# Kernel tuning notes

Measured on AMD Instinct MI355X. Metric: run time of the kernel, lower is better.

Reference implementation:

```python
import jax, jax.numpy as jnp
from jax import lax
import numpy as np

Z, Y, X = 41, 256, 256  # sparse_shape = grid_size[::-1]
N_VOX = 60000
C_IN = 4
DN = ('NCDHW', 'OIDHW', 'NCDHW')


def _conv(x, w, stride=(1, 1, 1), pad=1):
    return lax.conv_general_dilated(x, w, stride, [(pad, pad)] * 3, dimension_numbers=DN)


def _tconv(x, w, stride=(2, 2, 2), pad=1, outpad=(0, 0, 0)):
    # torch ConvTranspose3d (weight [Cin,Cout,k,k,k]) == conv with lhs dilation,
    # spatially-flipped, in/out-swapped kernel, padding (k-1-p, k-1-p+output_padding)
    wt = jnp.flip(jnp.swapaxes(w, 0, 1), axis=(2, 3, 4))
    padding = [(2 - pad, 2 - pad + op) for op in outpad]  # k=3
    return lax.conv_general_dilated(x, wt, (1, 1, 1), padding, lhs_dilation=stride, dimension_numbers=DN)


def _bn_relu(y, s, b, m):
    # eval-mode BN folded into per-channel scale/shift, then ReLU, then restrict
    # to the sparse active-site mask (spconv only stores features at active sites)
    return jax.nn.relu(y * s[None, :, None, None, None] + b[None, :, None, None, None]) * m


def _forward(feats, params, coords, batch_size):
    (w1, s1, b1, w2a, s2a, b2a, w2b, s2b, b2b, w3a, s3a, b3a, w3b, s3b, b3b,
     w4a, s4a, b4a, w4b, s4b, b4b, w5a, s5a, b5a, w5b, s5b, b5b) = params
    B = batch_size
    bi, zi, yi, xi = coords[:, 0], coords[:, 1], coords[:, 2], coords[:, 3]
    dense = jnp.zeros((B, C_IN, Z, Y, X), feats.dtype).at[bi, :, zi, yi, xi].set(feats)
    m0 = jnp.zeros((B, 1, Z, Y, X), feats.dtype).at[bi, 0, zi, yi, xi].set(1.0)
    one = jnp.ones((1, 1, 3, 3, 3), feats.dtype)
    # conv1: SparseConv3d k3 s1 p1 -> active set dilates
    m1 = (_conv(m0, one) > 0).astype(feats.dtype)
    x = _bn_relu(_conv(dense, w1), s1, b1, m1)
    # conv2: SparseConv3d s2 + SubMConv3d (mask unchanged for subm)
    m2 = (_conv(m1, one, (2, 2, 2)) > 0).astype(feats.dtype)
    x = _bn_relu(_conv(x, w2a, (2, 2, 2)), s2a, b2a, m2)
    x = _bn_relu(_conv(x, w2b), s2b, b2b, m2)
    # conv3
    m3 = (_conv(m2, one, (2, 2, 2)) > 0).astype(feats.dtype)
    x = _bn_relu(_conv(x, w3a, (2, 2, 2)), s3a, b3a, m3)
    x = _bn_relu(_conv(x, w3b), s3b, b3b, m3)
    # deconv4: SparseConvTranspose3d s2 + subm
    m4 = (_tconv(m3, one) > 0).astype(feats.dtype)
    x = _bn_relu(_tconv(x, w4a), s4a, b4a, m4)
    x = _bn_relu(_conv(x, w4b), s4b, b4b, m4)
    # deconv5: output_padding (0,3,3) restores full Y/X resolution
    m5 = (_tconv(m4, one, outpad=(0, 3, 3)) > 0).astype(feats.dtype)
    x = _bn_relu(_tconv(x, w5a, outpad=(0, 3, 3)), s5a, b5a, m5)
    x = _bn_relu(_conv(x, w5b), s5b, b5b, m5)
    return x  # dense [B, 32, Z, Y, X]; zeros at inactive sites


def setup_inputs() -> dict:
    rng = np.random.default_rng(0)
    flat = rng.choice(Z * Y * X, size=N_VOX, replace=False)
    zi = (flat // (Y * X)).astype(np.int32)
    rem = flat % (Y * X)
    yi = (rem // X).astype(np.int32)
    xi = (rem % X).astype(np.int32)
    coords = np.stack([np.zeros(N_VOX, np.int32), zi, yi, xi], axis=1)

    def w(o, i):
        return jnp.asarray((rng.standard_normal((o, i, 3, 3, 3)) * 0.05).astype(np.float32))

    def scale(c):
        return jnp.asarray(rng.uniform(0.5, 1.5, c).astype(np.float32))

    def shift(c):
        return jnp.asarray((rng.standard_normal(c) * 0.1).astype(np.float32))

    return {
        'occ_voxel_features': jnp.asarray(rng.standard_normal((N_VOX, C_IN)).astype(np.float32)),
        'occ_voxel_coords': jnp.asarray(coords),
        'batch_size': 1,
        'w1': w(16, 4), 's1': scale(16), 'b1': shift(16),
        'w2a': w(32, 16), 's2a': scale(32), 'b2a': shift(32),
        'w2b': w(32, 32), 's2b': scale(32), 'b2b': shift(32),
        'w3a': w(64, 32), 's3a': scale(64), 'b3a': shift(64),
        'w3b': w(64, 64), 's3b': scale(64), 'b3b': shift(64),
        'w4a': w(64, 32), 's4a': scale(32), 'b4a': shift(32),  # transpose weight [Cin,Cout,...]
        'w4b': w(32, 32), 's4b': scale(32), 'b4b': shift(32),
        'w5a': w(32, 32), 's5a': scale(32), 'b5a': shift(32),
        'w5b': w(32, 32), 's5b': scale(32), 'b5b': shift(32),
    }


def reference(occ_voxel_features, occ_voxel_coords, batch_size,
              w1, s1, b1, w2a, s2a, b2a, w2b, s2b, b2b,
              w3a, s3a, b3a, w3b, s3b, b3b,
              w4a, s4a, b4a, w4b, s4b, b4b,
              w5a, s5a, b5a, w5b, s5b, b5b):
    params = (w1, s1, b1, w2a, s2a, b2a, w2b, s2b, b2b, w3a, s3a, b3a, w3b, s3b, b3b,
              w4a, s4a, b4a, w4b, s4b, b4b, w5a, s5a, b5a, w5b, s5b, b5b)
    return _forward(occ_voxel_features, params, occ_voxel_coords, batch_size)
```

## Files before the change

### kernel.cpp

```cpp
#include <hip/hip_runtime.h>
#include <hip/hip_bf16.h>
#include <stdint.h>

namespace {

constexpr int Z0 = 41, Y0 = 256, X0 = 256;
constexpr int Z2 = 21, Y2 = 128, X2 = 128;
constexpr int Z3 = 11, Y3 = 64,  X3 = 64;
constexpr int Z4 = 21, Y4 = 127, X4 = 127;
constexpr int NV0 = Z0 * Y0 * X0;
constexpr int NV2 = Z2 * Y2 * X2;
constexpr int NV3 = Z3 * Y3 * X3;
constexpr int NV4 = Z4 * Y4 * X4;

constexpr int ZP0 = 43, YP0 = 258, XP0 = 258; constexpr int NP0 = ZP0 * YP0 * XP0;
constexpr int ZP2 = 23, YP2 = 130, XP2 = 130; constexpr int NP2 = ZP2 * YP2 * XP2;
constexpr int ZP3 = 13, YP3 = 66,  XP3 = 66;  constexpr int NP3 = ZP3 * YP3 * XP3;
constexpr int ZP4 = 23, YP4 = 129, XP4 = 129; constexpr int NP4 = ZP4 * YP4 * XP4;

using bf16 = __hip_bfloat16;
typedef __attribute__((ext_vector_type(8))) short s16x8;
typedef __attribute__((ext_vector_type(4))) float f32x4;
typedef __attribute__((ext_vector_type(16))) float f32x16;
typedef __attribute__((ext_vector_type(4))) unsigned u32x4;

__device__ inline unsigned f2b(float f) {
    return (unsigned)__builtin_bit_cast(unsigned short, __float2bfloat16(f));
}

__device__ inline int xcd_swz(int bid, int nwg) {
    int q = nwg >> 3, r = nwg & 7;
    int x = bid & 7, j = bid >> 3;
    return (x < r ? x * (q + 1) : r * (q + 1) + (x - r) * q) + j;
}

__device__ inline void glds16(const bf16* g, void* l) {
    __builtin_amdgcn_global_load_lds(
        (const __attribute__((address_space(1))) void*)g,
        (__attribute__((address_space(3))) void*)l, 16, 0, 0);
}

__global__ __launch_bounds__(256) void sentinel_k(float* out) { out[0] = 12345.0f; }

__global__ __launch_bounds__(256) void scatter_k(const float* __restrict__ feats,
                                                 const int* __restrict__ coords,
                                                 bf16* __restrict__ dense,
                                                 uint8_t* __restrict__ m0, int n) {
    int v = blockIdx.x * 256 + threadIdx.x;
    if (v >= n) return;
    int z = coords[v * 4 + 1], y = coords[v * 4 + 2], x = coords[v * 4 + 3];
    m0[(z * Y0 + y) * X0 + x] = 1;
    int pp = ((z + 1) * YP0 + (y + 1)) * XP0 + (x + 1);
    uint2 u;
    u.x = f2b(feats[v * 4 + 0]) | (f2b(feats[v * 4 + 1]) << 16);
    u.y = f2b(feats[v * 4 + 2]) | (f2b(feats[v * 4 + 3]) << 16);
    *(uint2*)(dense + (size_t)pp * 4) = u;
}

template <int C>
__global__ __launch_bounds__(256) void halo_zero_k(bf16* __restrict__ buf,
                                                   int Zi, int Yi, int Xi,
                                                   int Zp, int Yp, int Xp) {
    int i = blockIdx.x * 256 + threadIdx.x;
    int tot = Zp * Yp * Xp;
    if (i >= tot) return;
    int x = i % Xp; int t = i / Xp; int y = t % Yp; int z = t / Yp;
    bool halo = (z < 1) | (z > Zi) | (y < 1) | (y > Yi) | (x < 1) | (x > Xi);
    if (!halo) return;
    uint4 zz = make_uint4(0, 0, 0, 0);
    uint4* p = (uint4*)(buf + (size_t)i * C);
#pragma unroll
    for (int j = 0; j < C / 8; ++j) p[j] = zz;
}

__global__ __launch_bounds__(256) void repack_frag_k(const float* __restrict__ w,
                                                     bf16* __restrict__ wf,
                                                     int CIN, int COUT, int TRANS) {
    int NT = COUT / 16, KT = CIN / 32;
    int i = blockIdx.x * 256 + threadIdx.x;
    int total = 27 * NT * KT * 64;
    if (i >= total) return;
    int lane = i & 63; int t = i >> 6;
    int kt = t % KT; t /= KT; int nt = t % NT; int tap = t / NT;
    int co = nt * 16 + (lane & 15);
    int ci0 = kt * 32 + (lane >> 4) * 8;
    unsigned e[8];
#pragma unroll
    for (int j = 0; j < 8; ++j) {
        int ci = ci0 + j;
        int src = TRANS ? ((ci * COUT + co) * 27 + tap) : ((co * CIN + ci) * 27 + tap);
        e[j] = f2b(w[src]);
    }
    uint4 u;
    u.x = e[0] | (e[1] << 16); u.y = e[2] | (e[3] << 16);
    u.z = e[4] | (e[5] << 16); u.w = e[6] | (e[7] << 16);
    ((uint4*)wf)[i] = u;
}

__global__ __launch_bounds__(256) void repack_frag32_k(const float* __restrict__ w,
                                                       bf16* __restrict__ wf) {
    int i = blockIdx.x * 256 + threadIdx.x;
    if (i >= 27 * 2 * 64) return;
    int lane = i & 63; int t2 = i >> 6;
    int ks = t2 & 1; int tap = t2 >> 1;
    int co = lane & 31; int h = lane >> 5;
    unsigned e[8];
#pragma unroll
    for (int j = 0; j < 8; ++j) {
        int cin = ks * 16 + h * 8 + j;
        e[j] = f2b(w[(co * 32 + cin) * 27 + tap]);
    }
    uint4 u;
    u.x = e[0] | (e[1] << 16); u.y = e[2] | (e[3] << 16);
    u.z = e[4] | (e[5] << 16); u.w = e[6] | (e[7] << 16);
    ((uint4*)wf)[i] = u;
}

__global__ __launch_bounds__(256) void repack_frag_c16_k(const float* __restrict__ w,
                                                         bf16* __restrict__ wf) {
    int i = blockIdx.x * 256 + threadIdx.x;
    int total = 14 * 2 * 64;
    if (i >= total) return;
    int lane = i & 63; int t = i >> 6;
    int nt = t & 1; int p = t >> 1;
    int lg = lane >> 4, lr = lane & 15;
    int co = nt * 16 + lr;
    unsigned e[8];
#pragma unroll
    for (int j = 0; j < 8; ++j) {
        int tap = 2 * p + (lg >> 1);
        int ci = (lg & 1) * 8 + j;
        e[j] = (tap < 27) ? f2b(w[(co * 16 + ci) * 27 + tap]) : 0u;
    }
    uint4 u;
    u.x = e[0] | (e[1] << 16); u.y = e[2] | (e[3] << 16);
    u.z = e[4] | (e[5] << 16); u.w = e[6] | (e[7] << 16);
    ((uint4*)wf)[i] = u;
}

__global__ __launch_bounds__(256) void repack_frag_l1_k(const float* __restrict__ w,
                                                        bf16* __restrict__ wf) {
    int i = blockIdx.x * 256 + threadIdx.x;
    if (i >= 256) return;
    int lane = i & 63, kb = i >> 6;
    int lg = lane >> 4, lr = lane & 15;
    unsigned e[8];
#pragma unroll
    for (int j = 0; j < 8; ++j) {
        int tap = kb * 8 + lg * 2 + (j >> 2);
        int ci = j & 3;
        e[j] = (tap < 27) ? f2b(w[(lr * 4 + ci) * 27 + tap]) : 0u;
    }
    uint4 u;
    u.x = e[0] | (e[1] << 16); u.y = e[2] | (e[3] << 16);
    u.z = e[4] | (e[5] << 16); u.w = e[6] | (e[7] << 16);
    ((uint4*)wf)[i] = u;
}

__global__ __launch_bounds__(256) void dilate_k(const uint8_t* __restrict__ in,
                                                uint8_t* __restrict__ out,
                                                int Zi, int Yi, int Xi,
                                                int Zo, int Yo, int Xo, int stride) {
    int idx = blockIdx.x * 256 + threadIdx.x;
    int total = Zo * Yo * Xo;
    if (idx >= total) return;
    int x = idx % Xo; int t = idx / Xo; int y = t % Yo; int z = t / Yo;
    int YX = Yi * Xi;
    uint8_t r = 0;
    for (int kz = 0; kz < 3; ++kz) {
        int zi = z * stride + kz - 1;
        if ((unsigned)zi >= (unsigned)Zi) continue;
        for (int ky = 0; ky < 3; ++ky) {
            int yi = y * stride + ky - 1;
            if ((unsigned)yi >= (unsigned)Yi) continue;
            for (int kx = 0; kx < 3; ++kx) {
                int xi = x * stride + kx - 1;
                if ((unsigned)xi >= (unsigned)Xi) continue;
                r |= in[zi * YX + yi * Xi + xi];
            }
        }
    }
    out[idx] = r ? 1 : 0;
}

__global__ __launch_bounds__(256) void dilate4_k(const uint8_t* __restrict__ in,
                                                 uint8_t* __restrict__ out,
                                                 int Z, int Y, int X) {
    int ngx = X >> 2;
    int g = blockIdx.x * 256 + threadIdx.x;
    int total = Z * Y * ngx;
    if (g >= total) return;
    int gx = g % ngx; int t = g / ngx; int y = t % Y; int z = t / Y;
    const int YX = Y * X;
    unsigned r = 0;
    for (int kz = 0; kz < 3; ++kz) {
        int zi = z + kz - 1;
        if ((unsigned)zi >= (unsigned)Z) continue;
        for (int ky = 0; ky < 3; ++ky) {
            int yi = y + ky - 1;
            if ((unsigned)yi >= (unsigned)Y) continue;
            const unsigned* rw = (const unsigned*)(in + zi * YX + yi * X);
            unsigned u1 = rw[gx];
            unsigned u0 = gx ? rw[gx - 1] : 0u;
            unsigned u2 = (gx + 1 < ngx) ? rw[gx + 1] : 0u;
            r |= u1 | ((u1 << 8) | (u0 >> 24)) | ((u1 >> 8) | (u2 << 24));
        }
    }
    r |= r >> 4; r |= r >> 2; r |= r >> 1; r &= 0x01010101u;
    ((unsigned*)out)[g] = r;
}

__global__ __launch_bounds__(256) void tdilate_k(const uint8_t* __restrict__ in,
                                                 uint8_t* __restrict__ out,
                                                 int Zi, int Yi, int Xi,
                                                 int Zo, int Yo, int Xo) {
    int idx = blockIdx.x * 256 + threadIdx.x;
    int total = Zo * Yo * Xo;
    if (idx >= total) return;
    int x = idx % Xo; int t = idx / Xo; int y = t % Yo; int z = t / Yo;
    int YX = Yi * Xi;
    uint8_t r = 0;
    for (int kz = 0; kz < 3; ++kz) {
        int tz = z + 1 - kz;
        if (tz & 1) continue;
        int zi = tz >> 1;
        if ((unsigned)zi >= (unsigned)Zi) continue;
        for (int ky = 0; ky < 3; ++ky) {
            int ty = y + 1 - ky;
            if (ty & 1) continue;
            int yi = ty >> 1;
            if ((unsigned)yi >= (unsigned)Yi) continue;
            for (int kx = 0; kx < 3; ++kx) {
                int tx = x + 1 - kx;
                if (tx & 1) continue;
                int xi = tx >> 1;
                if ((unsigned)xi >= (unsigned)Xi) continue;
                r |= in[zi * YX + yi * Xi + xi];
            }
        }
    }
    out[idx] = r ? 1 : 0;
}

__global__ __launch_bounds__(256) void tdilate4_k(const uint8_t* __restrict__ in,
                                                  uint8_t* __restrict__ out,
                                                  int Zi, int Yi, int Xi,
                                                  int Zo, int Yo, int Xo) {
    int ngx = Xo >> 2;
    int g = blockIdx.x * 256 + threadIdx.x;
    int total = Zo * Yo * ngx;
    if (g >= total) return;
    int gx = g % ngx; int t = g / ngx; int y = t % Yo; int z = t / Yo;
    int YX = Yi * Xi;
    int j0 = gx * 2;
    unsigned r0 = 0, r1 = 0, r2 = 0, r3 = 0;
    for (int kz = 0; kz < 3; ++kz) {
        int tz = z + 1 - kz;
        if (tz & 1) continue;
        int zi = tz >> 1;
        if ((unsigned)zi >= (unsigned)Zi) continue;
        for (int ky = 0; ky < 3; ++ky) {
            int ty = y + 1 - ky;
            if (ty & 1) continue;
            int yi = ty >> 1;
            if ((unsigned)yi >= (unsigned)Yi) continue;
            const uint8_t* rp = in + zi * YX + yi * Xi;
            unsigned b0 = (j0 < Xi) ? rp[j0] : 0u;
            unsigned b1 = (j0 + 1 < Xi) ? rp[j0 + 1] : 0u;
            unsigned b2 = (j0 + 2 < Xi) ? rp[j0 + 2] : 0u;
            r0 |= b0; r1 |= b0 | b1; r2 |= b1; r3 |= b1 | b2;
        }
    }
    unsigned rr = (r0 ? 1u : 0u) | (r1 ? 0x100u : 0u) | (r2 ? 0x10000u : 0u) | (r3 ? 0x1000000u : 0u);
    ((unsigned*)out)[g] = rr;
}

__global__ __launch_bounds__(512, 2) void conv_roll_k(
    const bf16* __restrict__ in, const bf16* __restrict__ wfrag,
    const float* __restrict__ scale, const float* __restrict__ shift,
    const uint8_t* __restrict__ mask, float* __restrict__ outf) {
    constexpr int ROWB = 2176;
    constexpr int SLABB = 24576;
    __shared__ uint4 ring4[5 * SLABB / 16];
    char* ring = (char*)ring4;

    const int bid = xcd_swz(blockIdx.x, gridDim.x);
    const int tx = bid & 7, ty = bid >> 3;
    const int y0 = ty * 8, x0 = tx * 32;

    const int tid = threadIdx.x;
    const int w = tid >> 6, lane = tid & 63;
    const int vx = lane & 31, h = lane >> 5;
    const int yr = w;

#pragma unroll
    for (int k = 0; k < 7; ++k) {
        int i = tid + k * 512;
        if (i < 27 * 2 * 64) {
            glds16(wfrag + (size_t)(k * 512 + w * 64 + lane) * 8,
                   ring + (k * 512 + w * 64) * 16);
        }
    }
    asm volatile("s_waitcnt vmcnt(0)" ::: "memory");
    __syncthreads();

    u32x4 breg[27][2];
#pragma unroll
    for (int t = 0; t < 27; ++t) {
        breg[t][0] = *(const u32x4*)(ring + (t * 2 + 0) * 1024 + lane * 16);
        breg[t][1] = *(const u32x4*)(ring + (t * 2 + 1) * 1024 + lane * 16);
    }
    __syncthreads();

    int soff[3];
#pragma unroll
    for (int k = 0; k < 3; ++k) {
        int i = tid + k * 512;
        int ii = i < 1360 ? i : 0;
        int row = ii / 136, c = ii - row * 136;
        int ks = c / 68, r2 = c - ks * 68, hh = r2 / 34, v = r2 - hh * 34;
        soff[k] = ((y0 + row) * XP0 + (x0 + v)) * 32 + (2 * ks + hh) * 8;
    }
    auto stagefn = [&](int p, char* slab) {
        int zs = p < ZP0 ? p : ZP0 - 1;
        const bf16* pb = in + (size_t)zs * ((size_t)YP0 * XP0 * 32);
        glds16(pb + soff[0], slab + w * 1024);
        glds16(pb + soff[1], slab + w * 1024 + 8192);
        glds16(pb + soff[2], slab + w * 1024 + 16384);
    };

    int asw[3];
#pragma unroll
    for (int dx = 0; dx < 3; ++dx) asw[dx] = h * 544 + (vx + dx) * 16;

    const float sc = scale[vx], sh = shift[vx];

    stagefn(0, ring);
    stagefn(1, ring + SLABB);
    stagefn(2, ring + 2 * SLABB);
    stagefn(3, ring + 3 * SLABB);
    stagefn(4, ring + 4 * SLABB);
    asm volatile("s_waitcnt vmcnt(0)" ::: "memory");
    __builtin_amdgcn_s_barrier();

    int s0 = 0;
    for (int z = 0; z < Z0; ++z) {
        const int s1 = s0 + 1 < 5 ? s0 + 1 : 0;
        const int s2 = s1 + 1 < 5 ? s1 + 1 : 0;
        const char* sl0 = ring + s0 * SLABB;
        const char* sl1 = ring + s1 * SLABB;
        const char* sl2 = ring + s2 * SLABB;

        f32x16 acc;
#pragma unroll
        for (int i = 0; i < 16; ++i) acc[i] = 0.f;

#pragma unroll
        for (int dz = 0; dz < 3; ++dz) {
            const char* slab = dz == 0 ? sl0 : (dz == 1 ? sl1 : sl2);
#pragma unroll
            for (int dy = 0; dy < 3; ++dy) {
                const char* rowp = slab + (yr + dy) * ROWB;
#pragma unroll
                for (int dx = 0; dx < 3; ++dx) {
                    const int tap = dz * 9 + dy * 3 + dx;
                    u32x4 a0 = *(const u32x4*)(rowp + asw[dx]);
                    u32x4 a1 = *(const u32x4*)(rowp + 1088 + asw[dx]);
                    acc = __builtin_amdgcn_mfma_f32_32x32x16_bf16(
                        __builtin_bit_cast(s16x8, a0),
                        __builtin_bit_cast(s16x8, breg[tap][0]), acc, 0, 0, 0);
                    acc = __builtin_amdgcn_mfma_f32_32x32x16_bf16(
                        __builtin_bit_cast(s16x8, a1),
                        __builtin_bit_cast(s16x8, breg[tap][1]), acc, 0, 0, 0);
                }
            }
        }

        const uint8_t* mrow = mask + ((size_t)z * Y0 + (y0 + yr)) * X0 + x0 + 4 * h;
        unsigned mq0 = *(const unsigned*)(mrow);
        unsigned mq1 = *(const unsigned*)(mrow + 8);
        unsigned mq2 = *(const unsigned*)(mrow + 16);
        unsigned mq3 = *(const unsigned*)(mrow + 24);

        const size_t obase = (size_t)vx * NV0 + ((size_t)z * Y0 + (y0 + yr)) * X0 + x0 + 4 * h;
#pragma unroll
        for (int q = 0; q < 4; ++q) {
            unsigned mq = q == 0 ? mq0 : (q == 1 ? mq1 : (q == 2 ? mq2 : mq3));
            f32x4 o;
#pragma unroll
            for (int r = 0; r < 4; ++r) {
                float m = (float)((mq >> (8 * r)) & 1);
                o[r] = fmaxf(fmaf(acc[q * 4 + r], sc, sh), 0.f) * m;
            }
            *(f32x4*)(outf + obase + 8 * q) = o;
        }

        __builtin_amdgcn_s_barrier();
        stagefn(z + 5, ring + s0 * SLABB);
        asm volatile("s_waitcnt vmcnt(11)" ::: "memory");
        s0 = s1;
    }
}

__global__ __launch_bounds__(256, 3) void tconv_roll_k(
    const bf16* __restrict__ in, const bf16* __restrict__ wfrag,
    const float* __restrict__ scale, const float* __restrict__ shift,
    const uint8_t* __restrict__ mask, bf16* __restrict__ out,
    int Zo, int Yo, int Xo, int Zi, int Ypi, int Xpi, int Ypo, int Xpo, int nx) {
    constexpr int ROWB = 34 * 64;
    constexpr int SLABB = 3 * ROWB;
    __shared__ uint4 ring4[4 * SLABB / 16];
    char* ring = (char*)ring4;

    const int oct = blockIdx.y;
    const int pz = oct >> 2, py = (oct >> 1) & 1, px = oct & 1;
    const int Zq = (Zo - pz + 1) >> 1;

    const int bid = xcd_swz(blockIdx.x, gridDim.x);
    const int tx = bid % nx, ty = bid / nx;
    const int yq0 = ty * 2, xq0 = tx * 32;

    const int tid = threadIdx.x;
    const int w = tid >> 6, lane = tid & 63;
    const int lg = lane >> 4, lr = lane & 15;
    const int yr = w >> 1, xh = w & 1;

    const int kz0 = pz ? 0 : 1, dzo0 = pz ? 1 : 0;
    const int ky0 = py ? 0 : 1, dyo0 = py ? 1 : 0;
    const int kx0 = px ? 0 : 1, dxo0 = px ? 1 : 0;

    auto stagefn = [&](int p, int slot) {
        if (w < 3) {
            int zs = p < Zi ? p : Zi - 1;
            char* slab = ring + slot * SLABB + w * ROWB;
            const bf16* pb = in + ((size_t)(zs + 1) * Ypi + (yq0 + 1 + w)) * (size_t)Xpi * 32
                                + (size_t)(xq0 + 1) * 32;
            int u0 = lane;      glds16(pb + (u0 ^ ((u0 >> 3) & 7)) * 8, slab);
            int u1 = 64 + lane; glds16(pb + (u1 ^ ((u1 >> 3) & 7)) * 8, slab + 1024);
            if (lane < 8) { int u2 = 128 + lane; glds16(pb + u2 * 8, slab + 2048); }
        }
    };

    const uint4* gw = (const uint4*)wfrag;
    uint4 breg[2][2][2][2];
#pragma unroll
    for (int iz = 0; iz < 2; ++iz) {
        int kz = iz ? 2 : kz0;
#pragma unroll
        for (int iy = 0; iy < 2; ++iy) {
            int ky = iy ? 2 : ky0;
#pragma unroll
            for (int ix = 0; ix < 2; ++ix) {
                int kx = ix ? 2 : kx0;
                int tap = kz * 9 + ky * 3 + kx;
                breg[iz][iy][ix][0] = gw[(tap * 2 + 0) * 64 + lane];
                breg[iz][iy][ix][1] = gw[(tap * 2 + 1) * 64 + lane];
            }
        }
    }

    int b0 = (xh * 16 + lr + dxo0) * 64 + lg * 16;
    int b1 = (xh * 16 + lr) * 64 + lg * 16;
    const int aswA = b0 ^ (((b0 >> 7) & 7) << 4);
    const int aswB = b1 ^ (((b1 >> 7) & 7) << 4);
    const int rowA = (yr + dyo0) * ROWB;
    const int rowB = yr * ROWB;

    const float sc0 = scale[lr], sh0 = shift[lr];
    const float sc1 = scale[16 + lr], sh1 = shift[16 + lr];

    const int yout = 2 * (yq0 + yr) + py;
    const int xb = 2 * (xq0 + xh * 16 + lg * 4) + px;

    stagefn(0, 0); stagefn(1, 1); stagefn(2, 2);
    uint2 mv;
    mv = *(const uint2*)(mask + ((size_t)pz * Yo + yout) * Xo + (xb - px));
    asm volatile("s_waitcnt vmcnt(0)" ::: "memory");
    __builtin_amdgcn_s_barrier();

    int rs0 = 0, wslot = 3;
    for (int zq = 0; zq < Zq; ++zq) {
        uint2 nv;
        {
            int zqn = (zq + 1 < Zq) ? zq + 1 : Zq - 1;
            nv = *(const uint2*)(mask + ((size_t)(2 * zqn + pz) * Yo + yout) * Xo + (xb - px));
        }
        stagefn(zq + 3, wslot);

        int rs1 = rs0 + 1 < 4 ? rs0 + 1 : 0;
        const char* sl_0 = ring + rs0 * SLABB;
        const char* sl_1 = ring + rs1 * SLABB;
        const char* slz0 = pz ? sl_1 : sl_0;
        const char* slz1 = sl_0;

        f32x4 acc0 = (f32x4){0, 0, 0, 0}, acc1 = (f32x4){0, 0, 0, 0};
#pragma unroll
        for (int iz = 0; iz < 2; ++iz) {
            if (iz > pz) continue;
            const char* slab = iz ? slz1 : slz0;
#pragma unroll
            for (int iy = 0; iy < 2; ++iy) {
                if (iy > py) continue;
                const char* rowp = slab + (iy ? rowB : rowA);
#pragma unroll
                for (int ix = 0; ix < 2; ++ix) {
                    if (ix > px) continue;
                    uint4 a = *(const uint4*)(rowp + (ix ? aswB : aswA));
                    acc0 = __builtin_amdgcn_mfma_f32_16x16x32_bf16(
                        __builtin_bit_cast(s16x8, a),
                        __builtin_bit_cast(s16x8, breg[iz][iy][ix][0]), acc0, 0, 0, 0);
                    acc1 = __builtin_amdgcn_mfma_f32_16x16x32_bf16(
                        __builtin_bit_cast(s16x8, a),
                        __builtin_bit_cast(s16x8, breg[iz][iy][ix][1]), acc1, 0, 0, 0);
                }
            }
        }

        const int zout = 2 * zq + pz;
        const size_t opdbase = ((size_t)(zout + 1) * Ypo + (yout + 1)) * Xpo;
#pragma unroll
        for (int r = 0; r < 4; ++r) {
            unsigned word = (r < 2) ? mv.x : mv.y;
            float m = (float)((word >> (px * 8 + (r & 1) * 16)) & 1);
            float v0 = fmaxf(fmaf(acc0[r], sc0, sh0), 0.f) * m;
            float v1 = fmaxf(fmaf(acc1[r], sc1, sh1), 0.f) * m;
            size_t opd = opdbase + (size_t)(xb + 2 * r + 1);
            out[opd * 32 + lr]      = __float2bfloat16(v0);
            out[opd * 32 + 16 + lr] = __float2bfloat16(v1);
        }

        asm volatile("s_waitcnt vmcnt(20)" ::: "memory");
        __builtin_amdgcn_s_barrier();
        rs0 = rs1;
        wslot = wslot + 1 < 4 ? wslot + 1 : 0;
        mv = nv;
    }
}

template <bool FINAL>
__global__ __launch_bounds__(512, 4) void conv_lds_k(
    const bf16* __restrict__ in, const bf16* __restrict__ wfrag,
    const float* __restrict__ scale, const float* __restrict__ shift,
    const uint8_t* __restrict__ mask, bf16* __restrict__ out, float* __restrict__ outf,
    int Zo, int Yo, int Xo, int Ypi, int Xpi, int Ypo, int Xpo, int nx, int ny) {
    constexpr int ROWB = 34 * 64;
    __shared__ uint4 tile4[36 * ROWB / 16];
    char* tile = (char*)tile4;

    const int No = Zo * Yo * Xo;
    const int bid = xcd_swz(blockIdx.x, gridDim.x);
    int tx = bid % nx; int tt = bid / nx; int ty = tt % ny; int tz = tt / ny;
    const int z0 = tz * 4, y0 = ty * 4, x0 = tx * 32;

    const int tid = threadIdx.x;
    const int w = tid >> 6, lane = tid & 63, lg = lane >> 4, lr = lane & 15;

    int anywork;
    {
        int row = tid >> 5, xl = tid & 31;
        int zz = z0 + (row >> 2), yy = y0 + (row & 3), xx = x0 + xl;
        int ok = (zz < Zo) && (yy < Yo) && (xx < Xo) && mask[((size_t)zz * Yo + yy) * Xo + xx];
        anywork = __syncthreads_or(ok);
    }

    f32x4 acc[4][2];
#pragma unroll
    for (int s = 0; s < 4; ++s) { acc[s][0] = (f32x4){0,0,0,0}; acc[s][1] = (f32x4){0,0,0,0}; }

    if (anywork) {
        const int lsw = (lane ^ ((lane >> 3) & 7)) * 8;
        for (int rr = w; rr < 36; rr += 8) {
            int dz = rr / 6, dy = rr % 6;
            const bf16* g = in + ((size_t)(z0 + dz) * Ypi + (y0 + dy)) * Xpi * 32 + (size_t)x0 * 32;
            char* l = tile + rr * ROWB;
            glds16(g + lsw, l);
            glds16(g + 512 + lsw, l + 1024);
            if (lane < 8) glds16(g + 1024 + lane * 8, l + 2048);
        }
        asm volatile("s_waitcnt vmcnt(0)" ::: "memory");
        __syncthreads();

        int rbB[4], bsw[4][3];
#pragma unroll
        for (int s = 0; s < 4; ++s) {
            int lrow = 2 * w + (s >> 1);
            rbB[s] = ((lrow >> 2) * 6 + (lrow & 3)) * ROWB;
            int xpart = (s & 1) * 16 + lr;
#pragma unroll
            for (int dx = 0; dx < 3; ++dx) {
                int b = (xpart + dx) * 64 + lg * 16;
                bsw[s][dx] = b ^ (((b >> 7) & 7) << 4);
            }
        }

        const uint4* gw = (const uint4*)wfrag;
#pragma unroll 1
        for (int dz = 0; dz < 3; ++dz) {
#pragma unroll
            for (int dy = 0; dy < 3; ++dy) {
                const int rowoff = (dz * 6 + dy) * ROWB;
#pragma unroll
                for (int dx = 0; dx < 3; ++dx) {
                    const int tap = dz * 9 + dy * 3 + dx;
                    uint4 b0 = gw[(tap * 2 + 0) * 64 + lane];
                    uint4 b1 = gw[(tap * 2 + 1) * 64 + lane];
                    uint4 ua[4];
#pragma unroll
                    for (int s = 0; s < 4; ++s)
                        ua[s] = *(const uint4*)(tile + rbB[s] + rowoff + bsw[s][dx]);
#pragma unroll
                    for (int s = 0; s < 4; ++s) {
                        acc[s][0] = __builtin_amdgcn_mfma_f32_16x16x32_bf16(
                            __builtin_bit_cast(s16x8, ua[s]),
                            __builtin_bit_cast(s16x8, b0), acc[s][0], 0, 0, 0);
                        acc[s][1] = __builtin_amdgcn_mfma_f32_16x16x32_bf16(
                            __builtin_bit_cast(s16x8, ua[s]),
                            __builtin_bit_cast(s16x8, b1), acc[s][1], 0, 0, 0);
                    }
                }
            }
        }
    }

#pragma unroll
    for (int s = 0; s < 4; ++s) {
        int lrow = 2 * w + (s >> 1);
        int zz = z0 + (lrow >> 2), yy = y0 + (lrow & 3);
        int xv = x0 + (s & 1) * 16 + lg * 4;
        bool rowok = (zz < Zo) && (yy < Yo);
        if (!rowok) continue;
        size_t idx0 = ((size_t)zz * Yo + yy) * Xo + xv;
        float mm[4];
#pragma unroll
        for (int r = 0; r < 4; ++r)
            mm[r] = (xv + r < Xo && mask[idx0 + r]) ? 1.f : 0.f;
        if constexpr (FINAL) {
#pragma unroll
            for (int nt = 0; nt < 2; ++nt) {
                int co = nt * 16 + lr;
                float sc = scale[co], sh = shift[co];
                f32x4 o;
#pragma unroll
                for (int r = 0; r < 4; ++r)
                    o[r] = fmaxf(fmaf(acc[s][nt][r], sc, sh), 0.f) * mm[r];
                if (xv + 3 < Xo) {
                    *(f32x4*)(outf + (size_t)co * No + idx0) = o;
                } else {
#pragma unroll
                    for (int r = 0; r < 4; ++r)
                        if (xv + r < Xo) outf[(size_t)co * No + idx0 + r] = o[r];
                }
            }
        } else {
            int opd = ((zz + 1) * Ypo + (yy + 1)) * Xpo + (xv + 1);
#pragma unroll
            for (int nt = 0; nt < 2; ++nt) {
                int co = nt * 16 + lr;
                float sc = scale[co], sh = shift[co];
#pragma unroll
                for (int r = 0; r < 4; ++r) {
                    if (xv + r >= Xo) continue;
                    float yv = fmaxf(fmaf(acc[s][nt][r], sc, sh), 0.f) * mm[r];
                    out[(size_t)(opd + r) * 32 + co] = __float2bfloat16(yv);
                }
            }
        }
    }
}

template <int CIN, int COUT, int STRIDE, int BLK, bool FINAL>
__global__ __launch_bounds__(BLK, ((CIN <= 32 && COUT <= 32) ? 4 : 2)) void conv_mfma_k(
    const bf16* __restrict__ in, const bf16* __restrict__ wfrag,
    const float* __restrict__ scale, const float* __restrict__ shift,
    const uint8_t* __restrict__ mask, bf16* __restrict__ out, float* __restrict__ outf,
    int Zo, int Yo, int Xo, int Ypi, int Xpi, int Ypo, int Xpo) {
    constexpr int NT = COUT / 16;
    constexpr int KT = CIN / 32;
    const int No = Zo * Yo * Xo;
    const int bid = xcd_swz(blockIdx.x, gridDim.x);
    const int tid = threadIdx.x;
    const int wv = tid >> 6, lane = tid & 63;
    const int lg = lane >> 4, lr = lane & 15;
    const int v0 = bid * BLK + wv * 64;
    if (v0 >= No) return;

    int vm = v0 + lane;
    bool mw = (vm < No) && (mask[vm] != 0);
    const bool anywork = (__ballot(mw) != 0ull);

    f32x4 acc[4][NT];
#pragma unroll
    for (int s = 0; s < 4; ++s)
#pragma unroll
        for (int nt = 0; nt < NT; ++nt) acc[s][nt] = (f32x4){0.f, 0.f, 0.f, 0.f};

    const uint4* gw = (const uint4*)wfrag;

    if (anywork) {
        int pA[4];
#pragma unroll
        for (int s = 0; s < 4; ++s) {
            int vr = v0 + s * 16 + lr;
            if (vr >= No) vr = 0;
// ... 169 lines not shown
    if (v0 >= Nq) return;

    bool mw = false;
    {
        int q = v0 + lane;
        if (q < Nq) {
            int zq = q / YXq; int rr = q - zq * YXq; int yq = rr / Xq; int xq = rr - yq * Xq;
            int zz = 2 * zq + pz, yy = 2 * yq + py, xx = 2 * xq + px;
            mw = mask[(zz * Yo + yy) * Xo + xx] != 0;
        }
    }
    const bool anywork = (__ballot(mw) != 0ull);

    f32x4 acc[4][NT];
#pragma unroll
    for (int s = 0; s < 4; ++s)
#pragma unroll
        for (int nt = 0; nt < NT; ++nt) acc[s][nt] = (f32x4){0.f, 0.f, 0.f, 0.f};

    const uint4* gw = (const uint4*)wfrag;

    if (anywork) {
        int pA[4];
#pragma unroll
        for (int s = 0; s < 4; ++s) {
            int q = v0 + s * 16 + lr;
            if (q >= Nq) q = 0;
            int zq = q / YXq; int rr = q - zq * YXq; int yq = rr / Xq; int xq = rr - yq * Xq;
            pA[s] = (((zq + 1) * Ypi + (yq + 1)) * Xpi + (xq + 1)) * CIN + lg * 8;
        }
        const int nkz = 1 + pz, nky = 1 + py, nkx = 1 + px;
        for (int iz = 0; iz < nkz; ++iz) {
            const int kz = pz ? (iz ? 2 : 0) : 1;
            const int dz = (pz && !iz) ? 1 : 0;
            for (int iy = 0; iy < nky; ++iy) {
                const int ky = py ? (iy ? 2 : 0) : 1;
                const int dy = (py && !iy) ? 1 : 0;
                for (int ix = 0; ix < nkx; ++ix) {
                    const int kx = px ? (ix ? 2 : 0) : 1;
                    const int dx = (px && !ix) ? 1 : 0;
                    const int tap = kz * 9 + ky * 3 + kx;
                    const int toff = ((dz * Ypi + dy) * Xpi + dx) * CIN;
                    uint4 ub[NT][KT];
#pragma unroll
                    for (int nt = 0; nt < NT; ++nt)
#pragma unroll
                        for (int kt = 0; kt < KT; ++kt)
                            ub[nt][kt] = gw[((tap * NT + nt) * KT + kt) * 64 + lane];
                    uint4 ua[4][KT];
#pragma unroll
                    for (int s = 0; s < 4; ++s)
#pragma unroll
                        for (int kt = 0; kt < KT; ++kt)
                            ua[s][kt] = *(const uint4*)(in + pA[s] + toff + kt * 32);
#pragma unroll
                    for (int s = 0; s < 4; ++s)
#pragma unroll
                        for (int kt = 0; kt < KT; ++kt)
#pragma unroll
                            for (int nt = 0; nt < NT; ++nt)
                                acc[s][nt] = __builtin_amdgcn_mfma_f32_16x16x32_bf16(
                                    __builtin_bit_cast(s16x8, ua[s][kt]),
                                    __builtin_bit_cast(s16x8, ub[nt][kt]), acc[s][nt], 0, 0, 0);
                }
            }
        }
    }

#pragma unroll
    for (int s = 0; s < 4; ++s) {
        const int vb = v0 + s * 16 + lg * 4;
        int opd[4]; float mm[4]; bool ok[4];
#pragma unroll
        for (int r = 0; r < 4; ++r) {
            int q = vb + r;
            ok[r] = q < Nq;
            int qc = ok[r] ? q : 0;
            int zq = qc / YXq; int rr = qc - zq * YXq; int yq = rr / Xq; int xq = rr - yq * Xq;
            int zz = 2 * zq + pz, yy = 2 * yq + py, xx = 2 * xq + px;
            mm[r] = (ok[r] && mask[(zz * Yo + yy) * Xo + xx]) ? 1.f : 0.f;
            opd[r] = ((zz + 1) * Ypo + (yy + 1)) * Xpo + (xx + 1);
        }
#pragma unroll
        for (int nt = 0; nt < NT; ++nt) {
            int co = nt * 16 + lr;
            float sc = scale[co], sh = shift[co];
#pragma unroll
            for (int r = 0; r < 4; ++r) {
                if (!ok[r]) continue;
                float yv = fmaxf(fmaf(acc[s][nt][r], sc, sh), 0.f) * mm[r];
                out[(size_t)opd[r] * COUT + co] = __float2bfloat16(yv);
            }
        }
    }
}

__global__ __launch_bounds__(256, 4) void conv_l1_mfma_k(
    const bf16* __restrict__ in, const bf16* __restrict__ wfrag,
    const float* __restrict__ scale, const float* __restrict__ shift,
    const uint8_t* __restrict__ mask, bf16* __restrict__ out,
    int Zo, int Yo, int Xo, int Ypi, int Xpi, int Ypo, int Xpo) {
    const int No = Zo * Yo * Xo;
    const int bid = xcd_swz(blockIdx.x, gridDim.x);
    const int tid = threadIdx.x;
    const int wv = tid >> 6, lane = tid & 63;
    const int lg = lane >> 4, lr = lane & 15;
    const int v0 = bid * 256 + wv * 64;
    if (v0 >= No) return;

    int vm = v0 + lane;
    bool mw = (vm < No) && (mask[vm] != 0);
    const bool anywork = (__ballot(mw) != 0ull);

    f32x4 acc[4];
#pragma unroll
    for (int s = 0; s < 4; ++s) acc[s] = (f32x4){0.f, 0.f, 0.f, 0.f};

    if (anywork) {
        const uint4* gw = (const uint4*)wfrag;
        uint4 bu[4];
#pragma unroll
        for (int kb = 0; kb < 4; ++kb) bu[kb] = gw[kb * 64 + lane];

        int vtf[4][2];
#pragma unroll
        for (int kb = 0; kb < 4; ++kb)
#pragma unroll
            for (int u = 0; u < 2; ++u) {
                int tp = kb * 8 + lg * 2 + u;
                int kz = tp / 9, r9 = tp - kz * 9, ky = r9 / 3, kx = r9 - ky * 3;
                vtf[kb][u] = (tp < 27) ? (((kz - 1) * Ypi + (ky - 1)) * Xpi + (kx - 1)) : 0;
            }

        int pV[4];
#pragma unroll
        for (int s = 0; s < 4; ++s) {
            int vr = v0 + s * 16 + lr;
            if (vr >= No) vr = 0;
            int zz = vr / (Yo * Xo); int rr = vr - zz * (Yo * Xo);
            int yy = rr / Xo; int xx = rr - yy * Xo;
            pV[s] = ((zz + 1) * Ypi + (yy + 1)) * Xpi + (xx + 1);
        }

#pragma unroll
        for (int kb = 0; kb < 4; ++kb) {
#pragma unroll
            for (int s = 0; s < 4; ++s) {
                uint2 a0 = *(const uint2*)(in + (size_t)(pV[s] + vtf[kb][0]) * 4);
                uint2 a1 = *(const uint2*)(in + (size_t)(pV[s] + vtf[kb][1]) * 4);
                int4 ai; ai.x = a0.x; ai.y = a0.y; ai.z = a1.x; ai.w = a1.y;
                acc[s] = __builtin_amdgcn_mfma_f32_16x16x32_bf16(
                    __builtin_bit_cast(s16x8, ai),
                    __builtin_bit_cast(s16x8, bu[kb]), acc[s], 0, 0, 0);
            }
        }
    }

#pragma unroll
    for (int s = 0; s < 4; ++s) {
        const int vb = v0 + s * 16 + lg * 4;
        int co = lr;
        float sc = scale[co], sh = shift[co];
#pragma unroll
        for (int r = 0; r < 4; ++r) {
            int v = vb + r;
            if (v >= No) continue;
            float mm = mask[v] ? 1.f : 0.f;
            int zz = v / (Yo * Xo); int rr = v - zz * (Yo * Xo);
            int yy = rr / Xo; int xx = rr - yy * Xo;
            int opd = ((zz + 1) * Ypo + (yy + 1)) * Xpo + (xx + 1);
            float yv = fmaxf(fmaf(acc[s][r], sc, sh), 0.f) * mm;
            out[(size_t)opd * 16 + co] = __float2bfloat16(yv);
        }
    }
}

inline int nblk(int n) { return (n + 255) / 256; }
inline int cdiv(int a, int b) { return (a + b - 1) / b; }

}

extern "C" void kernel_launch(void* const* d_in, const int* in_sizes, int n_in,
                              void* d_out, int out_size, void* d_ws, size_t ws_size,
                              hipStream_t stream) {
    const float* feats = (const float*)d_in[0];
    const int* coords = (const int*)d_in[1];
    const int NVOX = in_sizes[0] / 4;

    const float *w1 = (const float*)d_in[3], *s1 = (const float*)d_in[4], *b1 = (const float*)d_in[5];
    const float *w2a = (const float*)d_in[6], *s2a = (const float*)d_in[7], *b2a = (const float*)d_in[8];
    const float *w2b = (const float*)d_in[9], *s2b = (const float*)d_in[10], *b2b = (const float*)d_in[11];
    const float *w3a = (const float*)d_in[12], *s3a = (const float*)d_in[13], *b3a = (const float*)d_in[14];
    const float *w3b = (const float*)d_in[15], *s3b = (const float*)d_in[16], *b3b = (const float*)d_in[17];
    const float *w4a = (const float*)d_in[18], *s4a = (const float*)d_in[19], *b4a = (const float*)d_in[20];
    const float *w4b = (const float*)d_in[21], *s4b = (const float*)d_in[22], *b4b = (const float*)d_in[23];
    const float *w5a = (const float*)d_in[24], *s5a = (const float*)d_in[25], *b5a = (const float*)d_in[26];
    const float *w5b = (const float*)d_in[27], *s5b = (const float*)d_in[28], *b5b = (const float*)d_in[29];

    char* ws = (char*)d_ws;
    size_t off = 0;
    auto alloc = [&](size_t bytes) -> void* {
        void* p = ws + off;
        off = (off + bytes + 255) & ~(size_t)255;
        return p;
    };

    uint8_t* m0 = (uint8_t*)alloc(NV0);
    uint8_t* m1 = (uint8_t*)alloc(NV0);
    uint8_t* m2 = (uint8_t*)alloc(NV2);
    uint8_t* m3 = (uint8_t*)alloc(NV3);
    uint8_t* m4 = (uint8_t*)alloc(NV4);
    uint8_t* m5 = (uint8_t*)alloc(NV0);

    bf16* slot0 = (bf16*)alloc((size_t)NP0 * 32 * 2);
    bf16* slot1 = (bf16*)alloc((size_t)NP0 * 16 * 2);

    bf16* dense0 = slot0;
    bf16* x1     = slot1;
    bf16* x2a    = slot0;
    bf16* x2b    = slot1;
    bf16* x3a    = slot0;
    bf16* x3b    = slot1;
    bf16* x4a    = slot0;
    bf16* x4b    = slot1;
    bf16* x5a    = slot0;

    bf16* wfL1 = (bf16*)alloc(4 * 64 * 8 * 2);
    bf16* wf2a = (bf16*)alloc((size_t)14 * 2 * 64 * 16);
    bf16* wf2b = (bf16*)alloc((size_t)27 * 2 * 1 * 64 * 16);
    bf16* wf3a = (bf16*)alloc((size_t)27 * 4 * 1 * 64 * 16);
    bf16* wf3b = (bf16*)alloc((size_t)27 * 4 * 2 * 64 * 16);
    bf16* wf4a = (bf16*)alloc((size_t)27 * 2 * 2 * 64 * 16);
    bf16* wf4b = (bf16*)alloc((size_t)27 * 2 * 1 * 64 * 16);
    bf16* wf5a = (bf16*)alloc((size_t)27 * 2 * 1 * 64 * 16);
    bf16* wf5b32 = (bf16*)alloc((size_t)27 * 2 * 64 * 16);
    alloc(20u << 20);

    if (off > ws_size) {
        sentinel_k<<<1, 256, 0, stream>>>((float*)d_out);
        return;
    }

    hipMemsetAsync(dense0, 0, (size_t)NP0 * 4 * 2, stream);
    hipMemsetAsync(m0, 0, NV0, stream);
    repack_frag_l1_k<<<1, 256, 0, stream>>>(w1, wfL1);
    repack_frag_c16_k<<<nblk(14 * 2 * 64), 256, 0, stream>>>(w2a, wf2a);
    repack_frag_k<<<nblk(27 * 2 * 64), 256, 0, stream>>>(w2b, wf2b, 32, 32, 0);
    repack_frag_k<<<nblk(27 * 4 * 64), 256, 0, stream>>>(w3a, wf3a, 32, 64, 0);
    repack_frag_k<<<nblk(27 * 8 * 64), 256, 0, stream>>>(w3b, wf3b, 64, 64, 0);
    repack_frag_k<<<nblk(27 * 4 * 64), 256, 0, stream>>>(w4a, wf4a, 64, 32, 1);
    repack_frag_k<<<nblk(27 * 2 * 64), 256, 0, stream>>>(w4b, wf4b, 32, 32, 0);
    repack_frag_k<<<nblk(27 * 2 * 64), 256, 0, stream>>>(w5a, wf5a, 32, 32, 1);
    repack_frag32_k<<<nblk(27 * 2 * 64), 256, 0, stream>>>(w5b, wf5b32);

    scatter_k<<<nblk(NVOX), 256, 0, stream>>>(feats, coords, dense0, m0, NVOX);

    dilate4_k<<<nblk(NV0 / 4), 256, 0, stream>>>(m0, m1, Z0, Y0, X0);
    halo_zero_k<16><<<nblk(NP0), 256, 0, stream>>>(x1, Z0, Y0, X0, ZP0, YP0, XP0);
    conv_l1_mfma_k<<<nblk(NV0), 256, 0, stream>>>(
        dense0, wfL1, s1, b1, m1, x1, Z0, Y0, X0, YP0, XP0, YP0, XP0);

    dilate_k<<<nblk(NV2), 256, 0, stream>>>(m1, m2, Z0, Y0, X0, Z2, Y2, X2, 2);
    halo_zero_k<32><<<nblk(NP2), 256, 0, stream>>>(x2a, Z2, Y2, X2, ZP2, YP2, XP2);
    conv_s2c16_k<<<nblk(NV2), 256, 0, stream>>>(
        x1, wf2a, s2a, b2a, m2, x2a, Z2, Y2, X2, YP0, XP0, YP2, XP2);
    halo_zero_k<32><<<nblk(NP2), 256, 0, stream>>>(x2b, Z2, Y2, X2, ZP2, YP2, XP2);
    {
        int nx = cdiv(X2, 32), ny = cdiv(Y2, 4), nz = cdiv(Z2, 4);
        conv_lds_k<false><<<nx * ny * nz, 512, 0, stream>>>(
            x2a, wf2b, s2b, b2b, m2, x2b, nullptr, Z2, Y2, X2, YP2, XP2, YP2, XP2, nx, ny);
    }

    dilate_k<<<nblk(NV3), 256, 0, stream>>>(m2, m3, Z2, Y2, X2, Z3, Y3, X3, 2);
    halo_zero_k<64><<<nblk(NP3), 256, 0, stream>>>(x3a, Z3, Y3, X3, ZP3, YP3, XP3);
    conv_mfma_k<32, 64, 2, 64, false><<<cdiv(NV3, 64), 64, 0, stream>>>(
        x2b, wf3a, s3a, b3a, m3, x3a, nullptr, Z3, Y3, X3, YP2, XP2, YP3, XP3);
    halo_zero_k<64><<<nblk(NP3), 256, 0, stream>>>(x3b, Z3, Y3, X3, ZP3, YP3, XP3);
    conv_mfma_k<64, 64, 1, 64, false><<<cdiv(NV3, 64), 64, 0, stream>>>(
        x3a, wf3b, s3b, b3b, m3, x3b, nullptr, Z3, Y3, X3, YP3, XP3, YP3, XP3);

    tdilate_k<<<nblk(NV4), 256, 0, stream>>>(m3, m4, Z3, Y3, X3, Z4, Y4, X4);
    halo_zero_k<32><<<nblk(NP4), 256, 0, stream>>>(x4a, Z4, Y4, X4, ZP4, YP4, XP4);
    {
        int maxNq = ((Z4 + 1) >> 1) * ((Y4 + 1) >> 1) * ((X4 + 1) >> 1);
        dim3 g(nblk(maxNq), 8);
        tconv_mfma_k<64, 32><<<g, 256, 0, stream>>>(
            x3b, wf4a, s4a, b4a, m4, x4a, Z4, Y4, X4, YP3, XP3, YP4, XP4);
    }
    halo_zero_k<32><<<nblk(NP2), 256, 0, stream>>>(x4b, Z4, Y4, X4, ZP2, YP2, XP2);
    {
        int nx = cdiv(X4, 32), ny = cdiv(Y4, 4), nz = cdiv(Z4, 4);
        conv_lds_k<false><<<nx * ny * nz, 512, 0, stream>>>(
            x4a, wf4b, s4b, b4b, m4, x4b, nullptr, Z4, Y4, X4, YP4, XP4, YP2, XP2, nx, ny);
    }

    tdilate4_k<<<nblk(NV0 / 4), 256, 0, stream>>>(m4, m5, Z4, Y4, X4, Z0, Y0, X0);
    halo_zero_k<32><<<nblk(NP0), 256, 0, stream>>>(x5a, Z0, Y0, X0, ZP0, YP0, XP0);
    {
        dim3 g((Y0 / 2 / 2) * (X0 / 2 / 32), 8);
        tconv_roll_k<<<g, 256, 0, stream>>>(
            x4b, wf5a, s5a, b5a, m5, x5a, Z0, Y0, X0, Z4, YP2, XP2, YP0, XP0, X0 / 2 / 32);
    }
    {
        conv_roll_k<<<(X0 / 32) * (Y0 / 8), 512, 0, stream>>>(
            x5a, wf5b32, s5b, b5b, m5, (float*)d_out);
    }
}
```

Baseline: 851.9 us.

## Restructure final conv to compute two output rows per wave and split depth

```diff
diff --git a/kernel.cpp b/kernel.cpp
--- a/kernel.cpp
+++ b/kernel.cpp
@@ -275,31 +275,33 @@
     ((unsigned*)out)[g] = rr;
 }
 
-__global__ __launch_bounds__(512, 2) void conv_roll_k(
+__global__ __launch_bounds__(256, 1) void conv_roll_k(
     const bf16* __restrict__ in, const bf16* __restrict__ wfrag,
     const float* __restrict__ scale, const float* __restrict__ shift,
     const uint8_t* __restrict__ mask, float* __restrict__ outf) {
     constexpr int ROWB = 2176;
     constexpr int SLABB = 24576;
-    __shared__ uint4 ring4[5 * SLABB / 16];
+    __shared__ uint4 ring4[4 * SLABB / 16];
     char* ring = (char*)ring4;
 
     const int bid = xcd_swz(blockIdx.x, gridDim.x);
-    const int tx = bid & 7, ty = bid >> 3;
+    const int tx = bid & 7;
+    const int t2 = bid >> 3;
+    const int ty = t2 & 31;
+    const int zs = t2 >> 5;
     const int y0 = ty * 8, x0 = tx * 32;
+    const int zlo = zs ? 21 : 0;
+    const int zcnt = zs ? 20 : 21;
 
     const int tid = threadIdx.x;
     const int w = tid >> 6, lane = tid & 63;
     const int vx = lane & 31, h = lane >> 5;
-    const int yr = w;
-
-#pragma unroll
-    for (int k = 0; k < 7; ++k) {
-        int i = tid + k * 512;
-        if (i < 27 * 2 * 64) {
-            glds16(wfrag + (size_t)(k * 512 + w * 64 + lane) * 8,
-                   ring + (k * 512 + w * 64) * 16);
-        }
+
+#pragma unroll
+    for (int k = 0; k < 14; ++k) {
+        int base = k * 256 + w * 64;
+        if (base < 27 * 2 * 64)
+            glds16(wfrag + (size_t)(base + lane) * 8, ring + base * 16);
     }
     asm volatile("s_waitcnt vmcnt(0)" ::: "memory");
     __syncthreads();
@@ -312,93 +314,109 @@
     }
     __syncthreads();
 
-    int soff[3];
-#pragma unroll
-    for (int k = 0; k < 3; ++k) {
-        int i = tid + k * 512;
+    int soff[6];
+#pragma unroll
+    for (int k = 0; k < 6; ++k) {
+        int i = tid + k * 256;
         int ii = i < 1360 ? i : 0;
         int row = ii / 136, c = ii - row * 136;
         int ks = c / 68, r2 = c - ks * 68, hh = r2 / 34, v = r2 - hh * 34;
         soff[k] = ((y0 + row) * XP0 + (x0 + v)) * 32 + (2 * ks + hh) * 8;
     }
     auto stagefn = [&](int p, char* slab) {
-        int zs = p < ZP0 ? p : ZP0 - 1;
-        const bf16* pb = in + (size_t)zs * ((size_t)YP0 * XP0 * 32);
-        glds16(pb + soff[0], slab + w * 1024);
-        glds16(pb + soff[1], slab + w * 1024 + 8192);
-        glds16(pb + soff[2], slab + w * 1024 + 16384);
+        int zp = p < ZP0 ? p : ZP0 - 1;
+        const bf16* pb = in + (size_t)zp * ((size_t)YP0 * XP0 * 32);
+#pragma unroll
+        for (int k = 0; k < 6; ++k)
+            glds16(pb + soff[k], slab + (k * 256 + w * 64) * 16);
     };
 
-    int asw[3];
-#pragma unroll
-    for (int dx = 0; dx < 3; ++dx) asw[dx] = h * 544 + (vx + dx) * 16;
+    int rb[4];
+#pragma unroll
+    for (int fr = 0; fr < 4; ++fr)
+        rb[fr] = (2 * w + fr) * ROWB + h * 544 + vx * 16;
 
     const float sc = scale[vx], sh = shift[vx];
 
-    stagefn(0, ring);
-    stagefn(1, ring + SLABB);
-    stagefn(2, ring + 2 * SLABB);
-    stagefn(3, ring + 3 * SLABB);
-    stagefn(4, ring + 4 * SLABB);
+    stagefn(zlo + 0, ring);
+    stagefn(zlo + 1, ring + SLABB);
+    stagefn(zlo + 2, ring + 2 * SLABB);
     asm volatile("s_waitcnt vmcnt(0)" ::: "memory");
     __builtin_amdgcn_s_barrier();
 
     int s0 = 0;
-    for (int z = 0; z < Z0; ++z) {
-        const int s1 = s0 + 1 < 5 ? s0 + 1 : 0;
-        const int s2 = s1 + 1 < 5 ? s1 + 1 : 0;
-        const char* sl0 = ring + s0 * SLABB;
-        const char* sl1 = ring + s1 * SLABB;
-        const char* sl2 = ring + s2 * SLABB;
-
-        f32x16 acc;
-#pragma unroll
-        for (int i = 0; i < 16; ++i) acc[i] = 0.f;
+    for (int zi = 0; zi < zcnt; ++zi) {
+        const int z = zlo + zi;
+        stagefn(z + 3, ring + ((s0 + 3) & 3) * SLABB);
+
+        unsigned mk0[4], mk1[4];
+        {
+            const uint8_t* mr0 = mask + ((size_t)z * Y0 + (y0 + 2 * w)) * X0 + x0 + 4 * h;
+            const uint8_t* mr1 = mr0 + X0;
+            mk0[0] = *(const unsigned*)(mr0);      mk0[1] = *(const unsigned*)(mr0 + 8);
+            mk0[2] = *(const unsigned*)(mr0 + 16); mk0[3] = *(const unsigned*)(mr0 + 24);
+            mk1[0] = *(const unsigned*)(mr1);      mk1[1] = *(const unsigned*)(mr1 + 8);
+            mk1[2] = *(const unsigned*)(mr1 + 16); mk1[3] = *(const unsigned*)(mr1 + 24);
+        }
+
+        const char* slp0 = ring + s0 * SLABB;
+        const char* slp1 = ring + ((s0 + 1) & 3) * SLABB;
+        const char* slp2 = ring + ((s0 + 2) & 3) * SLABB;
+
+        f32x16 acc0, acc1;
+#pragma unroll
+        for (int i = 0; i < 16; ++i) { acc0[i] = 0.f; acc1[i] = 0.f; }
 
 #pragma unroll
         for (int dz = 0; dz < 3; ++dz) {
-            const char* slab = dz == 0 ? sl0 : (dz == 1 ? sl1 : sl2);
-#pragma unroll
-            for (int dy = 0; dy < 3; ++dy) {
-                const char* rowp = slab + (yr + dy) * ROWB;
-#pragma unroll
-                for (int dx = 0; dx < 3; ++dx) {
-                    const int tap = dz * 9 + dy * 3 + dx;
-                    u32x4 a0 = *(const u32x4*)(rowp + asw[dx]);
-                    u32x4 a1 = *(const u32x4*)(rowp + 1088 + asw[dx]);
-                    acc = __builtin_amdgcn_mfma_f32_32x32x16_bf16(
-                        __builtin_bit_cast(s16x8, a0),
-                        __builtin_bit_cast(s16x8, breg[tap][0]), acc, 0, 0, 0);
-                    acc = __builtin_amdgcn_mfma_f32_32x32x16_bf16(
-                        __builtin_bit_cast(s16x8, a1),
-                        __builtin_bit_cast(s16x8, breg[tap][1]), acc, 0, 0, 0);
+            const char* slab = dz == 0 ? slp0 : (dz == 1 ? slp1 : slp2);
+#pragma unroll
+            for (int dx = 0; dx < 3; ++dx) {
+#pragma unroll
+                for (int ks = 0; ks < 2; ++ks) {
+                    const int ko = ks * 1088 + dx * 16;
+                    u32x4 a0 = *(const u32x4*)(slab + rb[0] + ko);
+                    u32x4 a1 = *(const u32x4*)(slab + rb[1] + ko);
+                    u32x4 a2 = *(const u32x4*)(slab + rb[2] + ko);
+                    u32x4 a3 = *(const u32x4*)(slab + rb[3] + ko);
+                    const int t0 = dz * 9 + 0 * 3 + dx;
+                    const int t1 = dz * 9 + 1 * 3 + dx;
+                    const int t2_ = dz * 9 + 2 * 3 + dx;
+                    acc0 = __builtin_amdgcn_mfma_f32_32x32x16_bf16(
+                        __builtin_bit_cast(s16x8, a0), __builtin_bit_cast(s16x8, breg[t0][ks]), acc0, 0, 0, 0);
+                    acc1 = __builtin_amdgcn_mfma_f32_32x32x16_bf16(
+                        __builtin_bit_cast(s16x8, a1), __builtin_bit_cast(s16x8, breg[t0][ks]), acc1, 0, 0, 0);
+                    acc0 = __builtin_amdgcn_mfma_f32_32x32x16_bf16(
+                        __builtin_bit_cast(s16x8, a1), __builtin_bit_cast(s16x8, breg[t1][ks]), acc0, 0, 0, 0);
+                    acc1 = __builtin_amdgcn_mfma_f32_32x32x16_bf16(
+                        __builtin_bit_cast(s16x8, a2), __builtin_bit_cast(s16x8, breg[t1][ks]), acc1, 0, 0, 0);
+                    acc0 = __builtin_amdgcn_mfma_f32_32x32x16_bf16(
+                        __builtin_bit_cast(s16x8, a2), __builtin_bit_cast(s16x8, breg[t2_][ks]), acc0, 0, 0, 0);
+                    acc1 = __builtin_amdgcn_mfma_f32_32x32x16_bf16(
+                        __builtin_bit_cast(s16x8, a3), __builtin_bit_cast(s16x8, breg[t2_][ks]), acc1, 0, 0, 0);
                 }
             }
         }
 
-        const uint8_t* mrow = mask + ((size_t)z * Y0 + (y0 + yr)) * X0 + x0 + 4 * h;
-        unsigned mq0 = *(const unsigned*)(mrow);
-        unsigned mq1 = *(const unsigned*)(mrow + 8);
-        unsigned mq2 = *(const unsigned*)(mrow + 16);
-        unsigned mq3 = *(const unsigned*)(mrow + 24);
-
-        const size_t obase = (size_t)vx * NV0 + ((size_t)z * Y0 + (y0 + yr)) * X0 + x0 + 4 * h;
+        const size_t ob0 = (size_t)vx * NV0 + ((size_t)z * Y0 + (y0 + 2 * w)) * X0 + x0 + 4 * h;
+        const size_t ob1 = ob0 + X0;
 #pragma unroll
         for (int q = 0; q < 4; ++q) {
-            unsigned mq = q == 0 ? mq0 : (q == 1 ? mq1 : (q == 2 ? mq2 : mq3));
-            f32x4 o;
+            f32x4 o0, o1;
 #pragma unroll
             for (int r = 0; r < 4; ++r) {
-                float m = (float)((mq >> (8 * r)) & 1);
-                o[r] = fmaxf(fmaf(acc[q * 4 + r], sc, sh), 0.f) * m;
-            }
-            *(f32x4*)(outf + obase + 8 * q) = o;
-        }
-
+                float m0 = (float)((mk0[q] >> (8 * r)) & 1);
+                float m1 = (float)((mk1[q] >> (8 * r)) & 1);
+                o0[r] = fmaxf(fmaf(acc0[q * 4 + r], sc, sh), 0.f) * m0;
+                o1[r] = fmaxf(fmaf(acc1[q * 4 + r], sc, sh), 0.f) * m1;
+            }
+            *(f32x4*)(outf + ob0 + 8 * q) = o0;
+            *(f32x4*)(outf + ob1 + 8 * q) = o1;
+        }
+
+        asm volatile("s_waitcnt vmcnt(8)" ::: "memory");
         __builtin_amdgcn_s_barrier();
-        stagefn(z + 5, ring + s0 * SLABB);
-        asm volatile("s_waitcnt vmcnt(11)" ::: "memory");
-        s0 = s1;
+        s0 = (s0 + 1) & 3;
     }
 }
 
@@ -1174,7 +1192,7 @@
             x4b, wf5a, s5a, b5a, m5, x5a, Z0, Y0, X0, Z4, YP2, XP2, YP0, XP0, X0 / 2 / 32);
     }
     {
-        conv_roll_k<<<(X0 / 32) * (Y0 / 8), 512, 0, stream>>>(
+        conv_roll_k<<<512, 256, 0, stream>>>(
             x5a, wf5b32, s5b, b5b, m5, (float*)d_out);
     }
 }
```

Result: faster. 797.9 us (-6.3%).
